# Kernel optimization log

Measured on AMD Instinct MI355X. Metric: run time of the kernel, lower is better.

Reference implementation:

```python
import jax, jax.numpy as jnp
import numpy as np

N, E, G, H, F_IN = 100_000, 3_200_000, 256, 16, 7
RRELU_SLOPE = (1.0 / 8.0 + 1.0 / 3.0) / 2.0  # eval-mode RReLU uses mean slope


def rrelu(x):
    return jnp.where(x >= 0, x, RRELU_SLOPE * x)


def gcn_conv(x, edge_index, edge_weight, W, b, n_nodes):
    """PyG GCNConv: add self-loops, symmetric norm, gather-matmul-scatter."""
    row, col = edge_index[0], edge_index[1]
    loop = jnp.arange(n_nodes)
    row = jnp.concatenate([row, loop])
    col = jnp.concatenate([col, loop])
    w = jnp.concatenate([edge_weight, jnp.ones((n_nodes,), x.dtype)])
    deg = jax.ops.segment_sum(w, col, num_segments=n_nodes)
    dis = jnp.where(deg > 0, jax.lax.rsqrt(jnp.maximum(deg, 1e-12)), 0.0)
    norm = dis[row] * w * dis[col]            # [E+N]
    h = x @ W                                  # [N, out]
    msg = h[row] * norm[:, None]               # gather + scale
    return jax.ops.segment_sum(msg, col, num_segments=n_nodes) + b


def max_pool_neighbor_x(x, edge_index, n_nodes):
    row, col = edge_index[0], edge_index[1]
    loop = jnp.arange(n_nodes)
    row = jnp.concatenate([row, loop])
    col = jnp.concatenate([col, loop])
    return jax.ops.segment_max(x[row], col, num_segments=n_nodes)


def setup_inputs() -> dict:
    key = jax.random.key(0)
    ks = jax.random.split(key, 12)
    x = jax.random.normal(ks[0], (N, F_IN), jnp.float32)
    edge_index = jax.random.randint(ks[1], (2, E), 0, N)
    edge_weights = jax.random.uniform(ks[2], (E,), jnp.float32)
    batch = (jnp.arange(N) * G) // N  # sorted, every graph non-empty
    s = 0.2
    W1 = jax.random.normal(ks[3], (F_IN, H), jnp.float32) * s
    b1 = jnp.zeros((H,), jnp.float32)
    W2 = jax.random.normal(ks[4], (H, H), jnp.float32) * s
    b2 = jnp.zeros((H,), jnp.float32)
    Wl1 = jax.random.normal(ks[5], (H, H), jnp.float32) * s
    bl1 = jax.random.normal(ks[6], (H,), jnp.float32) * s
    Wl3 = jax.random.normal(ks[7], (H, H), jnp.float32) * s
    bl3 = jax.random.normal(ks[8], (H,), jnp.float32) * s
    Wl4 = jax.random.normal(ks[9], (H, 1), jnp.float32) * s
    bl4 = jax.random.normal(ks[10], (1,), jnp.float32) * s
    return {"x": x, "edge_index": edge_index, "batch": batch,
            "edge_weights": edge_weights, "W1": W1, "b1": b1, "W2": W2,
            "b2": b2, "Wl1": Wl1, "bl1": bl1, "Wl3": Wl3, "bl3": bl3,
            "Wl4": Wl4, "bl4": bl4}


def reference(x, edge_index, batch, edge_weights, W1, b1, W2, b2,
              Wl1, bl1, Wl3, bl3, Wl4, bl4):
    h = gcn_conv(x, edge_index, edge_weights, W1, b1, N)
    h = max_pool_neighbor_x(h, edge_index, N)
    res = h
    h = gcn_conv(h, edge_index, jnp.ones((E,), h.dtype), W2, b2, N)
    h = jax.nn.relu(res + h)
    g = jax.ops.segment_max(h, batch, num_segments=G)  # global_max_pool
    res = g
    g = rrelu(res + (g @ Wl1 + bl1))
    res = g
    g = rrelu(res + (g @ Wl3 + bl3))
    # dropout p=0.5 in eval mode -> identity
    g = rrelu(g @ Wl4 + bl4)
    return g
```

## Files before the change

kernel.cpp:

```cpp
#include <hip/hip_runtime.h>
#include <hip/hip_fp16.h>
#include <math.h>

#define NN 100000
#define NE 3200000
#define NG 256
#define HD 16
#define FIN 7

#define RB 8
#define RSZ 256
#define NBUK 391
#define NBUKP 400
#define FB 512
#define CHUNK 6250
#define CH2 3125
#define SCB 8
#define LMASK 0x1FFFF

#define SEGN 32
#define SEGB 3125
#define NPW 8

#define PSTRIDE_B 10880
#define SCAP PSTRIDE_B

#define S_DEGW 16777216.0f
#define INV_S_DEGW 5.9604644775390625e-8f

static constexpr float SLOPE = 0.22916666666666666f;

__device__ __forceinline__ float rrelu_f(float a) {
    return a >= 0.f ? a : SLOPE * a;
}

__device__ __forceinline__ float h2f(unsigned short us) {
    __half h = *(__half*)&us;
    return __half2float(h);
}


__global__ __launch_bounds__(512) void k_hist(
        const int* __restrict__ col, int* __restrict__ hist) {
    __shared__ int bins[NBUK];
    for (int i = threadIdx.x; i < NBUK; i += 512) bins[i] = 0;
    __syncthreads();
    const int2* c2 = (const int2*)(col + blockIdx.x * CHUNK);
    for (int i = threadIdx.x; i < CH2; i += 512) {
        int2 v = c2[i];
        atomicAdd(&bins[v.x >> RB], 1);
        atomicAdd(&bins[v.y >> RB], 1);
    }
    __syncthreads();
    for (int i = threadIdx.x; i < NBUK; i += 512)
        hist[blockIdx.x * NBUKP + i] = bins[i];
}

__global__ __launch_bounds__(512) void k_scan_a(
        const int* __restrict__ hist, int* __restrict__ pre_t,
        int* __restrict__ tot) {
    __shared__ int s[SCB * (FB + 1)];
    int t = threadIdx.x;
    int c0 = blockIdx.x * SCB;
    for (int i = t; i < SCB * FB; i += 512) {
        int j = i >> 3, c = i & 7;
        int cc = c0 + c;
        s[c * (FB + 1) + j] = (cc < NBUK) ? hist[j * NBUKP + cc] : 0;
    }
    __syncthreads();
    int w = t >> 6, l = t & 63;
    int* sb = &s[w * (FB + 1)];
    int base = l * 8;
    int loc[8];
    int run = 0;
#pragma unroll
    for (int k = 0; k < 8; ++k) { loc[k] = run; run += sb[base + k]; }
    int inc = run;
#pragma unroll
    for (int d = 1; d < 64; d <<= 1) {
        int v = __shfl_up(inc, d, 64);
        if (l >= d) inc += v;
    }
    int excl = inc - run;
    int cc = c0 + w;
    if (cc < NBUK) {
#pragma unroll
        for (int k = 0; k < 8; ++k) sb[base + k] = excl + loc[k];
        if (l == 63) tot[cc] = inc;
    }
    __syncthreads();
    for (int i = t; i < SCB * FB; i += 512) {
        int j = i >> 3, c = i & 7;
        int cc2 = c0 + c;
        if (cc2 < NBUK) pre_t[j * NBUKP + cc2] = s[c * (FB + 1) + j];
    }
}

__global__ __launch_bounds__(512) void k_scan_b(
        const int* __restrict__ tot, int* __restrict__ bstart,
        unsigned* __restrict__ gbuf) {
    __shared__ int s[512];
    int t = threadIdx.x;
    for (int i = t; i < NG * HD; i += 512) gbuf[i] = 0u;
    int v = (t < NBUK) ? tot[t] : 0;
    s[t] = v;
    __syncthreads();
    for (int d = 1; d < 512; d <<= 1) {
        int add = (t >= d) ? s[t - d] : 0;
        __syncthreads();
        s[t] += add;
        __syncthreads();
    }
    if (t < NBUK) bstart[t + 1] = s[t];
    if (t == 0) bstart[0] = 0;
}

__global__ __launch_bounds__(512) void k_fill(
        const int* __restrict__ row, const int* __restrict__ col,
        const float* __restrict__ ew,
        const int* __restrict__ pre_t, const int* __restrict__ bstart,
        unsigned* __restrict__ sp, unsigned short* __restrict__ swh) {
    __shared__ int lcnt[NBUK];
    __shared__ int gofs[NBUK];
    __shared__ int part[512];
    __shared__ unsigned ssp[CHUNK];
    __shared__ unsigned short ssw[CHUNK];
    __shared__ unsigned short sbuk[CHUNK];
    int t = threadIdx.x;
    for (int i = t; i < NBUK; i += 512) {
        lcnt[i] = 0;
        gofs[i] = bstart[i] + pre_t[blockIdx.x * NBUKP + i];
    }
    __syncthreads();
    const int2* c2 = (const int2*)(col + blockIdx.x * CHUNK);
    const int2* r2 = (const int2*)(row + blockIdx.x * CHUNK);
    const float2* e2 = (const float2*)(ew + blockIdx.x * CHUNK);
    for (int i = t; i < CH2; i += 512) {
        int2 v = c2[i];
        atomicAdd(&lcnt[v.x >> RB], 1);
        atomicAdd(&lcnt[v.y >> RB], 1);
    }
    __syncthreads();
    int c = (t < NBUK) ? lcnt[t] : 0;
    part[t] = c;
    __syncthreads();
    for (int d = 1; d < 512; d <<= 1) {
        int add = (t >= d) ? part[t - d] : 0;
        __syncthreads();
        part[t] += add;
        __syncthreads();
    }
    if (t < NBUK) {
        int e = part[t] - c;
        gofs[t] -= e;
        lcnt[t] = e;
    }
    __syncthreads();
    for (int i = t; i < CH2; i += 512) {
        int2 cv = c2[i];
        int2 rv = r2[i];
        float2 wv = e2[i];
        {
            int b = cv.x >> RB;
            int s = atomicAdd(&lcnt[b], 1);
            ssp[s] = ((unsigned)(cv.x & (RSZ - 1)) << 17) | (unsigned)rv.x;
            __half hv = __float2half_rn(wv.x);
            ssw[s] = *(unsigned short*)&hv;
            sbuk[s] = (unsigned short)b;
        }
        {
            int b = cv.y >> RB;
            int s = atomicAdd(&lcnt[b], 1);
            ssp[s] = ((unsigned)(cv.y & (RSZ - 1)) << 17) | (unsigned)rv.y;
            __half hv = __float2half_rn(wv.y);
            ssw[s] = *(unsigned short*)&hv;
            sbuk[s] = (unsigned short)b;
        }
    }
    __syncthreads();
    for (int s = t; s < CHUNK; s += 512) {
        int g = s + gofs[sbuk[s]];
        sp[g] = ssp[s];
        swh[g] = ssw[s];
    }
}

__global__ __launch_bounds__(1024) void k_deg(
        const unsigned* __restrict__ sp, const unsigned short* __restrict__ swh,
        const int* __restrict__ bstart,
        const float* __restrict__ x, const float* __restrict__ W1,
        float* __restrict__ dis1, float* __restrict__ dis2,
        int* __restrict__ pstart, int* __restrict__ cnts,
        unsigned* __restrict__ h1h, unsigned* __restrict__ sp2) {
    __shared__ unsigned long long sdeg[RSZ];
    __shared__ float sdis[RSZ];
    __shared__ float sW1[FIN * HD];
    __shared__ int sscan[RSZ];
    __shared__ int lrank[RSZ];
    __shared__ unsigned sstage[SCAP];
    int t = threadIdx.x;
    if (t < FIN * HD) sW1[t] = W1[t];
    if (t < RSZ) sdeg[t] = 0ULL;
    __syncthreads();
    int s0 = bstart[blockIdx.x], s1 = bstart[blockIdx.x + 1];
    int j = s0 + t;
    for (; j + 3072 < s1; j += 4096) {
        unsigned e0 = sp[j], e1 = sp[j + 1024], e2 = sp[j + 2048], e3 = sp[j + 3072];
        float w0 = h2f(swh[j]), w1 = h2f(swh[j + 1024]);
        float w2 = h2f(swh[j + 2048]), w3 = h2f(swh[j + 3072]);
        atomicAdd(&sdeg[e0 >> 17], (1ULL << 32) |
                  (unsigned long long)(unsigned)__float2int_rn(w0 * S_DEGW));
        atomicAdd(&sdeg[e1 >> 17], (1ULL << 32) |
                  (unsigned long long)(unsigned)__float2int_rn(w1 * S_DEGW));
        atomicAdd(&sdeg[e2 >> 17], (1ULL << 32) |
                  (unsigned long long)(unsigned)__float2int_rn(w2 * S_DEGW));
        atomicAdd(&sdeg[e3 >> 17], (1ULL << 32) |
                  (unsigned long long)(unsigned)__float2int_rn(w3 * S_DEGW));
    }
    for (; j < s1; j += 1024) {
        unsigned e = sp[j];
        float w = h2f(swh[j]);
        atomicAdd(&sdeg[e >> 17], (1ULL << 32) |
                  (unsigned long long)(unsigned)__float2int_rn(w * S_DEGW));
    }
    __syncthreads();
    int node0 = blockIdx.x * RSZ;
    int s0p = blockIdx.x * PSTRIDE_B;
    int cnt_t = 0, pc_t = 0;
    if (t < RSZ) {
        cnt_t = (int)(sdeg[t] >> 32);
        pc_t = (cnt_t + 15) & ~15;
        sscan[t] = pc_t;
    }
    __syncthreads();
    for (int d = 1; d < RSZ; d <<= 1) {
        int add = (t < RSZ && t >= d) ? sscan[t - d] : 0;
        __syncthreads();
        if (t < RSZ) sscan[t] += add;
        __syncthreads();
    }
    if (t < RSZ) {
        int excl = sscan[t] - pc_t;
        lrank[t] = excl;
        if (node0 + t < NN) {
            pstart[node0 + t] = s0p + excl;
            cnts[node0 + t] = cnt_t;
            unsigned long long v = sdeg[t];
            float wsum = (float)(unsigned)(v & 0xFFFFFFFFULL) * INV_S_DEGW;
            float d1 = rsqrtf(wsum + 1.f);
            dis1[node0 + t] = d1;
            sdis[t] = d1;
            dis2[node0 + t] = rsqrtf((float)cnt_t + 1.f);
        }
        int pbase = excl + cnt_t;
        unsigned pv = (unsigned)(node0 + t);
        for (int k = cnt_t; k < pc_t; ++k) {
            int pos = pbase + (k - cnt_t);
            if (pos < SCAP) sstage[pos] = pv;
        }
    }
    __syncthreads();
    for (int k = s0 + t; k < s1; k += 1024) {
        unsigned e = sp[k];
        unsigned short wb = swh[k];
        int pos = atomicAdd(&lrank[e >> 17], 1);
        unsigned packed = ((unsigned)(wb & 0x7FFFu) << 17) | (e & LMASK);
        if (pos < SCAP) sstage[pos] = packed;
    }
    __syncthreads();
    int ptot = sscan[RSZ - 1];
    int lim = ptot < SCAP ? ptot : SCAP;
    for (int k = t; k < lim; k += 1024) sp2[s0p + k] = sstage[k];
    for (int i = t; i < RSZ * 8; i += 1024) {
        int ln = i >> 3, p = i & 7;
        int node = node0 + ln;
        if (node < NN) {
            float a0 = 0.f, a1 = 0.f;
#pragma unroll
            for (int k = 0; k < FIN; ++k) {
                float xv = x[node * FIN + k];
                a0 += xv * sW1[k * HD + 2 * p];
                a1 += xv * sW1[k * HD + 2 * p + 1];
            }
            float d = sdis[ln];
            __half2 hh = __floats2half2_rn(a0 * d, a1 * d);
            h1h[node * 8 + p] = *(unsigned*)&hh;
        }
    }
}

__global__ __launch_bounds__(256) void k_conv1(
        const unsigned* __restrict__ sp2, const int* __restrict__ pstart,
        const int* __restrict__ cnts,
        const unsigned* __restrict__ h1h, const float* __restrict__ dis1,
        const float* __restrict__ b1, unsigned* __restrict__ h1outh) {
    int t = threadIdx.x;
    int l = t & 63, w = t >> 6;
    int e = l >> 3, p = l & 7;
    float bb0 = b1[2 * p], bb1 = b1[2 * p + 1];
    int nwbase = blockIdx.x * SEGN + w * NPW;
    for (int nn = 0; nn < NPW; nn += 2) {
        int nodeA = __builtin_amdgcn_readfirstlane(nwbase + nn);
        int nodeB = nodeA + 1;
        int pA = pstart[nodeA], cA = cnts[nodeA];
        int pB = pstart[nodeB], cB = cnts[nodeB];
        int tA = (cA + 15) >> 4, tB = (cB + 15) >> 4;
        float dA = dis1[nodeA], dB = dis1[nodeB];
        unsigned shA = h1h[nodeA * 8 + p], shB = h1h[nodeB * 8 + p];
        float aA0 = 0.f, aA1 = 0.f, aB0 = 0.f, aB1 = 0.f;
        int jA = pA + e, jB = pB + e;
        while (tA > 0 || tB > 0) {
            if (tA > 0) {
                unsigned v0 = sp2[jA], v1 = sp2[jA + 8];
                unsigned g0 = h1h[(v0 & LMASK) * 8 + p];
                unsigned g1 = h1h[(v1 & LMASK) * 8 + p];
                float w0 = h2f((unsigned short)(v0 >> 17));
                float w1 = h2f((unsigned short)(v1 >> 17));
                float2 f0 = __half22float2(*(__half2*)&g0);
                float2 f1 = __half22float2(*(__half2*)&g1);
                aA0 += f0.x * w0 + f1.x * w1;
                aA1 += f0.y * w0 + f1.y * w1;
                jA += 16; --tA;
            }
            if (tB > 0) {
                unsigned v0 = sp2[jB], v1 = sp2[jB + 8];
                unsigned g0 = h1h[(v0 & LMASK) * 8 + p];
                unsigned g1 = h1h[(v1 & LMASK) * 8 + p];
                float w0 = h2f((unsigned short)(v0 >> 17));
                float w1 = h2f((unsigned short)(v1 >> 17));
                float2 f0 = __half22float2(*(__half2*)&g0);
                float2 f1 = __half22float2(*(__half2*)&g1);
                aB0 += f0.x * w0 + f1.x * w1;
                aB1 += f0.y * w0 + f1.y * w1;
                jB += 16; --tB;
            }
        }
        aA0 += __shfl_xor(aA0, 8);  aB0 += __shfl_xor(aB0, 8);
        aA1 += __shfl_xor(aA1, 8);  aB1 += __shfl_xor(aB1, 8);
        aA0 += __shfl_xor(aA0, 16); aB0 += __shfl_xor(aB0, 16);
        aA1 += __shfl_xor(aA1, 16); aB1 += __shfl_xor(aB1, 16);
        aA0 += __shfl_xor(aA0, 32); aB0 += __shfl_xor(aB0, 32);
        aA1 += __shfl_xor(aA1, 32); aB1 += __shfl_xor(aB1, 32);
        float2 sfA = __half22float2(*(__half2*)&shA);
        float2 sfB = __half22float2(*(__half2*)&shB);
        float rA0 = (aA0 + sfA.x) * dA + bb0;
        float rA1 = (aA1 + sfA.y) * dA + bb1;
        float rB0 = (aB0 + sfB.x) * dB + bb0;
        float rB1 = (aB1 + sfB.y) * dB + bb1;
        if (e == 0) {
            __half2 ha = __floats2half2_rn(rA0, rA1);
            h1outh[nodeA * 8 + p] = *(unsigned*)&ha;
            __half2 hb = __floats2half2_rn(rB0, rB1);
            h1outh[nodeB * 8 + p] = *(unsigned*)&hb;
        }
    }
}

__global__ __launch_bounds__(256) void k_pool_h2(
        const unsigned* __restrict__ sp2, const int* __restrict__ pstart,
        const int* __restrict__ cnts,
        const unsigned* __restrict__ h1outh, const float* __restrict__ W2,
        const float* __restrict__ dis2,
        float2* __restrict__ pool2, unsigned* __restrict__ h2sh) {
    int t = threadIdx.x;
    int l = t & 63, w = t >> 6;
    int e = l >> 3, p = l & 7;
    float w00 = W2[(2 * e) * HD + 2 * p],     w10 = W2[(2 * e + 1) * HD + 2 * p];
    float w01 = W2[(2 * e) * HD + 2 * p + 1], w11 = W2[(2 * e + 1) * HD + 2 * p + 1];
    int nwbase = blockIdx.x * SEGN + w * NPW;
    for (int nn = 0; nn < NPW; nn += 2) {
        int nodeA = __builtin_amdgcn_readfirstlane(nwbase + nn);
        int nodeB = nodeA + 1;
        int pA = pstart[nodeA], cA = cnts[nodeA];
        int pB = pstart[nodeB], cB = cnts[nodeB];
        int tA = (cA + 15) >> 4, tB = (cB + 15) >> 4;
        float dA = dis2[nodeA], dB = dis2[nodeB];
        unsigned shA = h1outh[nodeA * 8 + p], shB = h1outh[nodeB * 8 + p];
        float2 sfA = __half22float2(*(__half2*)&shA);
        float2 sfB = __half22float2(*(__half2*)&shB);
        float mA0 = sfA.x, mA1 = sfA.y;
        float mB0 = sfB.x, mB1 = sfB.y;
        int jA = pA + e, jB = pB + e;
        while (tA > 0 || tB > 0) {
            if (tA > 0) {
                unsigned v0 = sp2[jA], v1 = sp2[jA + 8];
                unsigned g0 = h1outh[(v0 & LMASK) * 8 + p];
                unsigned g1 = h1outh[(v1 & LMASK) * 8 + p];
                float2 f0 = __half22float2(*(__half2*)&g0);
                float2 f1 = __half22float2(*(__half2*)&g1);
                mA0 = fmaxf(mA0, fmaxf(f0.x, f1.x));
                mA1 = fmaxf(mA1, fmaxf(f0.y, f1.y));
                jA += 16; --tA;
            }
            if (tB > 0) {
                unsigned v0 = sp2[jB], v1 = sp2[jB + 8];
                unsigned g0 = h1outh[(v0 & LMASK) * 8 + p];
                unsigned g1 = h1outh[(v1 & LMASK) * 8 + p];
                float2 f0 = __half22float2(*(__half2*)&g0);
                float2 f1 = __half22float2(*(__half2*)&g1);
                mB0 = fmaxf(mB0, fmaxf(f0.x, f1.x));
                mB1 = fmaxf(mB1, fmaxf(f0.y, f1.y));
                jB += 16; --tB;
            }
        }
        mA0 = fmaxf(mA0, __shfl_xor(mA0, 8));  mB0 = fmaxf(mB0, __shfl_xor(mB0, 8));
        mA1 = fmaxf(mA1, __shfl_xor(mA1, 8));  mB1 = fmaxf(mB1, __shfl_xor(mB1, 8));
        mA0 = fmaxf(mA0, __shfl_xor(mA0, 16)); mB0 = fmaxf(mB0, __shfl_xor(mB0, 16));
        mA1 = fmaxf(mA1, __shfl_xor(mA1, 16)); mB1 = fmaxf(mB1, __shfl_xor(mB1, 16));
        mA0 = fmaxf(mA0, __shfl_xor(mA0, 32)); mB0 = fmaxf(mB0, __shfl_xor(mB0, 32));
        mA1 = fmaxf(mA1, __shfl_xor(mA1, 32)); mB1 = fmaxf(mB1, __shfl_xor(mB1, 32));
        if (e == 0) {
            pool2[nodeA * 8 + p] = make_float2(mA0, mA1);
            pool2[nodeB * 8 + p] = make_float2(mB0, mB1);
        }
        float pmA0 = __shfl(mA0, e), pmB0 = __shfl(mB0, e);
        float pmA1 = __shfl(mA1, e), pmB1 = __shfl(mB1, e);
        float aA0 = pmA0 * w00 + pmA1 * w10;
        float aA1 = pmA0 * w01 + pmA1 * w11;
        float aB0 = pmB0 * w00 + pmB1 * w10;
        float aB1 = pmB0 * w01 + pmB1 * w11;
        aA0 += __shfl_xor(aA0, 8);  aB0 += __shfl_xor(aB0, 8);
        aA1 += __shfl_xor(aA1, 8);  aB1 += __shfl_xor(aB1, 8);
        aA0 += __shfl_xor(aA0, 16); aB0 += __shfl_xor(aB0, 16);
        aA1 += __shfl_xor(aA1, 16); aB1 += __shfl_xor(aB1, 16);
        aA0 += __shfl_xor(aA0, 32); aB0 += __shfl_xor(aB0, 32);
        aA1 += __shfl_xor(aA1, 32); aB1 += __shfl_xor(aB1, 32);
        if (e == 0) {
            __half2 ha = __floats2half2_rn(aA0 * dA, aA1 * dA);
            h2sh[nodeA * 8 + p] = *(unsigned*)&ha;
            __half2 hb = __floats2half2_rn(aB0 * dB, aB1 * dB);
            h2sh[nodeB * 8 + p] = *(unsigned*)&hb;
        }
    }
}

__global__ __launch_bounds__(256) void k_conv2(
        const unsigned* __restrict__ sp2, const int* __restrict__ pstart,
        const int* __restrict__ cnts,
        const unsigned* __restrict__ h2sh, const float* __restrict__ dis2,
        const float2* __restrict__ pool2, const float* __restrict__ b2,
        unsigned* __restrict__ gbuf) {
    __shared__ unsigned sgmax[2 * HD];
    int t = threadIdx.x;
    if (t < 2 * HD) sgmax[t] = 0u;
    __syncthreads();
    int l = t & 63, w = t >> 6;
    int e = l >> 3, p = l & 7;
    float bb0 = b2[2 * p], bb1 = b2[2 * p + 1];
    int nbase = blockIdx.x * SEGN;
    int gbase = (int)(((unsigned long long)nbase * NG) / NN);
    int nwbase = nbase + w * NPW;
    for (int nn = 0; nn < NPW; nn += 2) {
        int nodeA = __builtin_amdgcn_readfirstlane(nwbase + nn);
        int nodeB = nodeA + 1;
        int pA = pstart[nodeA], cA = cnts[nodeA];
        int pB = pstart[nodeB], cB = cnts[nodeB];
        int tA = (cA + 15) >> 4, tB = (cB + 15) >> 4;
        int npadA = (tA << 4) - cA, npadB = (tB << 4) - cB;
        float dA = dis2[nodeA], dB = dis2[nodeB];
        unsigned shA = h2sh[nodeA * 8 + p], shB = h2sh[nodeB * 8 + p];
        float2 plA = pool2[nodeA * 8 + p], plB = pool2[nodeB * 8 + p];
        float aA0 = 0.f, aA1 = 0.f, aB0 = 0.f, aB1 = 0.f;
        int jA = pA + e, jB = pB + e;
        while (tA > 0 || tB > 0) {
            if (tA > 0) {
                unsigned v0 = sp2[jA], v1 = sp2[jA + 8];
                unsigned g0 = h2sh[(v0 & LMASK) * 8 + p];
                unsigned g1 = h2sh[(v1 & LMASK) * 8 + p];
                float2 f0 = __half22float2(*(__half2*)&g0);
                float2 f1 = __half22float2(*(__half2*)&g1);
                aA0 += f0.x + f1.x;
                aA1 += f0.y + f1.y;
                jA += 16; --tA;
            }
            if (tB > 0) {
                unsigned v0 = sp2[jB], v1 = sp2[jB + 8];
                unsigned g0 = h2sh[(v0 & LMASK) * 8 + p];
                unsigned g1 = h2sh[(v1 & LMASK) * 8 + p];
                float2 f0 = __half22float2(*(__half2*)&g0);
                float2 f1 = __half22float2(*(__half2*)&g1);
                aB0 += f0.x + f1.x;
                aB1 += f0.y + f1.y;
                jB += 16; --tB;
            }
        }
        aA0 += __shfl_xor(aA0, 8);  aB0 += __shfl_xor(aB0, 8);
        aA1 += __shfl_xor(aA1, 8);  aB1 += __shfl_xor(aB1, 8);
        aA0 += __shfl_xor(aA0, 16); aB0 += __shfl_xor(aB0, 16);
        aA1 += __shfl_xor(aA1, 16); aB1 += __shfl_xor(aB1, 16);
        aA0 += __shfl_xor(aA0, 32); aB0 += __shfl_xor(aB0, 32);
        aA1 += __shfl_xor(aA1, 32); aB1 += __shfl_xor(aB1, 32);
        float2 selfA = __half22float2(*(__half2*)&shA);
        float2 selfB = __half22float2(*(__half2*)&shB);
        float csA = 1.f - (float)npadA, csB = 1.f - (float)npadB;
        float rA0 = fmaxf(plA.x + (aA0 + csA * selfA.x) * dA + bb0, 0.f);
        float rA1 = fmaxf(plA.y + (aA1 + csA * selfA.y) * dA + bb1, 0.f);
        float rB0 = fmaxf(plB.x + (aB0 + csB * selfB.x) * dB + bb0, 0.f);
        float rB1 = fmaxf(plB.y + (aB1 + csB * selfB.y) * dB + bb1, 0.f);
        if (e == 0) {
            int lgA = (int)(((unsigned long long)nodeA * NG) / NN) - gbase;
            int lgB = (int)(((unsigned long long)nodeB * NG) / NN) - gbase;
            atomicMax(&sgmax[lgA * HD + 2 * p],     __float_as_uint(rA0));
            atomicMax(&sgmax[lgA * HD + 2 * p + 1], __float_as_uint(rA1));
            atomicMax(&sgmax[lgB * HD + 2 * p],     __float_as_uint(rB0));
            atomicMax(&sgmax[lgB * HD + 2 * p + 1], __float_as_uint(rB1));
        }
    }
    __syncthreads();
    if (t < 2 * HD) {
        int lg = t >> 4, f = t & 15;
        int gg = gbase + lg;
        unsigned m = sgmax[t];
        if (gg < NG && m > 0u) atomicMax(&gbuf[gg * HD + f], m);
    }
}

__global__ __launch_bounds__(256) void k_mlp(
        const float* __restrict__ gbuf,
        const float* __restrict__ Wl1, const float* __restrict__ bl1,
        const float* __restrict__ Wl3, const float* __restrict__ bl3,
        const float* __restrict__ Wl4, const float* __restrict__ bl4,
        float* __restrict__ out) {
    __shared__ float sW1[256], sW3[256], sW4[16], sb1[16], sb3[16];
    __shared__ float sb4;
    int tid = threadIdx.x;
    sW1[tid] = Wl1[tid];
    sW3[tid] = Wl3[tid];
    if (tid < 16) { sW4[tid] = Wl4[tid]; sb1[tid] = bl1[tid]; sb3[tid] = bl3[tid]; }
    if (tid == 0) sb4 = bl4[0];
    __syncthreads();

    float v[16], t1[16], t2[16];
#pragma unroll
    for (int f = 0; f < 16; ++f) v[f] = gbuf[tid * 16 + f];
#pragma unroll
    for (int f = 0; f < 16; ++f) {
        float a = sb1[f] + v[f];
#pragma unroll
        for (int k = 0; k < 16; ++k) a += v[k] * sW1[k * 16 + f];
        t1[f] = rrelu_f(a);
    }
#pragma unroll
    for (int f = 0; f < 16; ++f) {
        float a = sb3[f] + t1[f];
#pragma unroll
        for (int k = 0; k < 16; ++k) a += t1[k] * sW3[k * 16 + f];
        t2[f] = rrelu_f(a);
    }
    float o = sb4;
#pragma unroll
    for (int k = 0; k < 16; ++k) o += t2[k] * sW4[k];
    out[tid] = rrelu_f(o);
}

extern "C" void kernel_launch(void* const* d_in, const int* in_sizes, int n_in,
                              void* d_out, int out_size, void* d_ws, size_t ws_size,
                              hipStream_t stream) {
    const float* x   = (const float*)d_in[0];
    const int*   ei  = (const int*)  d_in[1];
    const float* ew  = (const float*)d_in[3];
    const float* W1  = (const float*)d_in[4];
    const float* b1  = (const float*)d_in[5];
    const float* W2  = (const float*)d_in[6];
    const float* b2  = (const float*)d_in[7];
    const float* Wl1 = (const float*)d_in[8];
    const float* bl1 = (const float*)d_in[9];
    const float* Wl3 = (const float*)d_in[10];
    const float* bl3 = (const float*)d_in[11];
    const float* Wl4 = (const float*)d_in[12];
    const float* bl4 = (const float*)d_in[13];
    const int* row = ei;
    const int* col = ei + NE;

    float* ws = (float*)d_ws;
    float* pool  = ws;
    float* dead  = pool + NN * HD;
    float* dis1  = dead + NN * HD;
    float* dis2  = dis1 + NN;
    int*   pstart = (int*)(dis2 + NN);
    int*   cnts  = pstart + NN;
    unsigned* gbuf = (unsigned*)(cnts + NN);
    unsigned* h1h    = gbuf   + NG * HD;
    unsigned* h1outh = h1h    + NN * 8;
    unsigned* h2sh   = h1outh + NN * 8;
    unsigned* sp     = h2sh   + NN * 8;
    unsigned short* swh = (unsigned short*)(sp + NE);
    unsigned* sp2    = (unsigned*)(swh + NE);
    int* tot    = (int*)(sp2 + (size_t)NBUK * PSTRIDE_B);
    int* bstart = tot + NBUK;
    int* hist   = (int*)pool;
    int* pre_t  = (int*)dead;

    k_hist     <<<FB, 512, 0, stream>>>(col, hist);
    k_scan_a   <<<(NBUK + SCB - 1) / SCB, 512, 0, stream>>>(hist, pre_t, tot);
    k_scan_b   <<<1, 512, 0, stream>>>(tot, bstart, gbuf);
    k_fill     <<<FB, 512, 0, stream>>>(row, col, ew, pre_t, bstart, sp, swh);
    k_deg      <<<NBUK, 1024, 0, stream>>>(sp, swh, bstart, x, W1,
                                           dis1, dis2, pstart, cnts, h1h, sp2);
    k_conv1    <<<SEGB, 256, 0, stream>>>(sp2, pstart, cnts, h1h, dis1,
                                          b1, h1outh);
    k_pool_h2  <<<SEGB, 256, 0, stream>>>(sp2, pstart, cnts, h1outh, W2, dis2,
                                          (float2*)pool, h2sh);
    k_conv2    <<<SEGB, 256, 0, stream>>>(sp2, pstart, cnts, h2sh, dis2,
                                          (const float2*)pool, b2, gbuf);
    k_mlp      <<<1, 256, 0, stream>>>((const float*)gbuf, Wl1, bl1, Wl3, bl3,
                                       Wl4, bl4, (float*)d_out);
}
```

Measured before the change: 252.5 us.

## Widen gather to 8-byte loads with 4 nodes per wavefront in CSR kernels

```diff
diff --git a/kernel.cpp b/kernel.cpp
--- a/kernel.cpp
+++ b/kernel.cpp
@@ -37,6 +37,12 @@
 __device__ __forceinline__ float h2f(unsigned short us) {
     __half h = *(__half*)&us;
     return __half2float(h);
+}
+
+__device__ __forceinline__ unsigned hmax2u(unsigned a, unsigned b) {
+    unsigned r;
+    asm volatile("v_pk_max_f16 %0, %1, %2" : "=v"(r) : "v"(a), "v"(b));
+    return r;
 }
 
 
@@ -295,63 +301,61 @@
         const unsigned* __restrict__ h1h, const float* __restrict__ dis1,
         const float* __restrict__ b1, unsigned* __restrict__ h1outh) {
     int t = threadIdx.x;
-    int l = t & 63, w = t >> 6;
-    int e = l >> 3, p = l & 7;
-    float bb0 = b1[2 * p], bb1 = b1[2 * p + 1];
-    int nwbase = blockIdx.x * SEGN + w * NPW;
-    for (int nn = 0; nn < NPW; nn += 2) {
-        int nodeA = __builtin_amdgcn_readfirstlane(nwbase + nn);
-        int nodeB = nodeA + 1;
-        int pA = pstart[nodeA], cA = cnts[nodeA];
-        int pB = pstart[nodeB], cB = cnts[nodeB];
-        int tA = (cA + 15) >> 4, tB = (cB + 15) >> 4;
-        float dA = dis1[nodeA], dB = dis1[nodeB];
-        unsigned shA = h1h[nodeA * 8 + p], shB = h1h[nodeB * 8 + p];
-        float aA0 = 0.f, aA1 = 0.f, aB0 = 0.f, aB1 = 0.f;
-        int jA = pA + e, jB = pB + e;
-        while (tA > 0 || tB > 0) {
-            if (tA > 0) {
-                unsigned v0 = sp2[jA], v1 = sp2[jA + 8];
-                unsigned g0 = h1h[(v0 & LMASK) * 8 + p];
-                unsigned g1 = h1h[(v1 & LMASK) * 8 + p];
-                float w0 = h2f((unsigned short)(v0 >> 17));
-                float w1 = h2f((unsigned short)(v1 >> 17));
-                float2 f0 = __half22float2(*(__half2*)&g0);
-                float2 f1 = __half22float2(*(__half2*)&g1);
-                aA0 += f0.x * w0 + f1.x * w1;
-                aA1 += f0.y * w0 + f1.y * w1;
-                jA += 16; --tA;
-            }
-            if (tB > 0) {
-                unsigned v0 = sp2[jB], v1 = sp2[jB + 8];
-                unsigned g0 = h1h[(v0 & LMASK) * 8 + p];
-                unsigned g1 = h1h[(v1 & LMASK) * 8 + p];
-                float w0 = h2f((unsigned short)(v0 >> 17));
-                float w1 = h2f((unsigned short)(v1 >> 17));
-                float2 f0 = __half22float2(*(__half2*)&g0);
-                float2 f1 = __half22float2(*(__half2*)&g1);
-                aB0 += f0.x * w0 + f1.x * w1;
-                aB1 += f0.y * w0 + f1.y * w1;
-                jB += 16; --tB;
-            }
-        }
-        aA0 += __shfl_xor(aA0, 8);  aB0 += __shfl_xor(aB0, 8);
-        aA1 += __shfl_xor(aA1, 8);  aB1 += __shfl_xor(aB1, 8);
-        aA0 += __shfl_xor(aA0, 16); aB0 += __shfl_xor(aB0, 16);
-        aA1 += __shfl_xor(aA1, 16); aB1 += __shfl_xor(aB1, 16);
-        aA0 += __shfl_xor(aA0, 32); aB0 += __shfl_xor(aB0, 32);
-        aA1 += __shfl_xor(aA1, 32); aB1 += __shfl_xor(aB1, 32);
-        float2 sfA = __half22float2(*(__half2*)&shA);
-        float2 sfB = __half22float2(*(__half2*)&shB);
-        float rA0 = (aA0 + sfA.x) * dA + bb0;
-        float rA1 = (aA1 + sfA.y) * dA + bb1;
-        float rB0 = (aB0 + sfB.x) * dB + bb0;
-        float rB1 = (aB1 + sfB.y) * dB + bb1;
-        if (e == 0) {
-            __half2 ha = __floats2half2_rn(rA0, rA1);
-            h1outh[nodeA * 8 + p] = *(unsigned*)&ha;
-            __half2 hb = __floats2half2_rn(rB0, rB1);
-            h1outh[nodeB * 8 + p] = *(unsigned*)&hb;
+    int wu = __builtin_amdgcn_readfirstlane(t >> 6);
+    int l = t & 63;
+    int e = l >> 2, p = l & 3;
+    float4 bb = ((const float4*)b1)[p];
+    const uint2* hv = (const uint2*)h1h;
+    int nwbase = blockIdx.x * SEGN + wu * NPW;
+    for (int nn = 0; nn < NPW; nn += 4) {
+        int nb = nwbase + nn;
+        int tC[4], jC[4];
+        float a0[4], a1[4], a2[4], a3[4];
+#pragma unroll
+        for (int c = 0; c < 4; ++c) {
+            int node = nb + c;
+            int pc = pstart[node];
+            tC[c] = (cnts[node] + 15) >> 4;
+            jC[c] = pc + e;
+            a0[c] = 0.f; a1[c] = 0.f; a2[c] = 0.f; a3[c] = 0.f;
+        }
+        while ((tC[0] | tC[1] | tC[2] | tC[3]) > 0) {
+#pragma unroll
+            for (int c = 0; c < 4; ++c) if (tC[c] > 0) {
+                unsigned v = sp2[jC[c]];
+                uint2 g = hv[(v & LMASK) * 4 + p];
+                float wv = h2f((unsigned short)(v >> 17));
+                float2 f0 = __half22float2(*(__half2*)&g.x);
+                float2 f1 = __half22float2(*(__half2*)&g.y);
+                a0[c] += f0.x * wv; a1[c] += f0.y * wv;
+                a2[c] += f1.x * wv; a3[c] += f1.y * wv;
+                jC[c] += 16; --tC[c];
+            }
+        }
+#pragma unroll
+        for (int c = 0; c < 4; ++c) {
+            int node = nb + c;
+#pragma unroll
+            for (int d = 4; d < 64; d <<= 1) {
+                a0[c] += __shfl_xor(a0[c], d);
+                a1[c] += __shfl_xor(a1[c], d);
+                a2[c] += __shfl_xor(a2[c], d);
+                a3[c] += __shfl_xor(a3[c], d);
+            }
+            float dd = dis1[node];
+            uint2 sh = hv[node * 4 + p];
+            float2 s0 = __half22float2(*(__half2*)&sh.x);
+            float2 s1 = __half22float2(*(__half2*)&sh.y);
+            float r0 = (a0[c] + s0.x) * dd + bb.x;
+            float r1 = (a1[c] + s0.y) * dd + bb.y;
+            float r2 = (a2[c] + s1.x) * dd + bb.z;
+            float r3 = (a3[c] + s1.y) * dd + bb.w;
+            if (e == 0) {
+                __half2 h01 = __floats2half2_rn(r0, r1);
+                __half2 h23 = __floats2half2_rn(r2, r3);
+                ((uint2*)h1outh)[node * 4 + p] =
+                    make_uint2(*(unsigned*)&h01, *(unsigned*)&h23);
+            }
         }
     }
 }
@@ -361,75 +365,59 @@
         const int* __restrict__ cnts,
         const unsigned* __restrict__ h1outh, const float* __restrict__ W2,
         const float* __restrict__ dis2,
-        float2* __restrict__ pool2, unsigned* __restrict__ h2sh) {
-    int t = threadIdx.x;
-    int l = t & 63, w = t >> 6;
-    int e = l >> 3, p = l & 7;
-    float w00 = W2[(2 * e) * HD + 2 * p],     w10 = W2[(2 * e + 1) * HD + 2 * p];
-    float w01 = W2[(2 * e) * HD + 2 * p + 1], w11 = W2[(2 * e + 1) * HD + 2 * p + 1];
-    int nwbase = blockIdx.x * SEGN + w * NPW;
-    for (int nn = 0; nn < NPW; nn += 2) {
-        int nodeA = __builtin_amdgcn_readfirstlane(nwbase + nn);
-        int nodeB = nodeA + 1;
-        int pA = pstart[nodeA], cA = cnts[nodeA];
-        int pB = pstart[nodeB], cB = cnts[nodeB];
-        int tA = (cA + 15) >> 4, tB = (cB + 15) >> 4;
-        float dA = dis2[nodeA], dB = dis2[nodeB];
-        unsigned shA = h1outh[nodeA * 8 + p], shB = h1outh[nodeB * 8 + p];
-        float2 sfA = __half22float2(*(__half2*)&shA);
-        float2 sfB = __half22float2(*(__half2*)&shB);
-        float mA0 = sfA.x, mA1 = sfA.y;
-        float mB0 = sfB.x, mB1 = sfB.y;
-        int jA = pA + e, jB = pB + e;
-        while (tA > 0 || tB > 0) {
-            if (tA > 0) {
-                unsigned v0 = sp2[jA], v1 = sp2[jA + 8];
-                unsigned g0 = h1outh[(v0 & LMASK) * 8 + p];
-                unsigned g1 = h1outh[(v1 & LMASK) * 8 + p];
-                float2 f0 = __half22float2(*(__half2*)&g0);
-                float2 f1 = __half22float2(*(__half2*)&g1);
-                mA0 = fmaxf(mA0, fmaxf(f0.x, f1.x));
-                mA1 = fmaxf(mA1, fmaxf(f0.y, f1.y));
-                jA += 16; --tA;
-            }
-            if (tB > 0) {
-                unsigned v0 = sp2[jB], v1 = sp2[jB + 8];
-                unsigned g0 = h1outh[(v0 & LMASK) * 8 + p];
-                unsigned g1 = h1outh[(v1 & LMASK) * 8 + p];
-                float2 f0 = __half22float2(*(__half2*)&g0);
-                float2 f1 = __half22float2(*(__half2*)&g1);
-                mB0 = fmaxf(mB0, fmaxf(f0.x, f1.x));
-                mB1 = fmaxf(mB1, fmaxf(f0.y, f1.y));
-                jB += 16; --tB;
-            }
-        }
-        mA0 = fmaxf(mA0, __shfl_xor(mA0, 8));  mB0 = fmaxf(mB0, __shfl_xor(mB0, 8));
-        mA1 = fmaxf(mA1, __shfl_xor(mA1, 8));  mB1 = fmaxf(mB1, __shfl_xor(mB1, 8));
-        mA0 = fmaxf(mA0, __shfl_xor(mA0, 16)); mB0 = fmaxf(mB0, __shfl_xor(mB0, 16));
-        mA1 = fmaxf(mA1, __shfl_xor(mA1, 16)); mB1 = fmaxf(mB1, __shfl_xor(mB1, 16));
-        mA0 = fmaxf(mA0, __shfl_xor(mA0, 32)); mB0 = fmaxf(mB0, __shfl_xor(mB0, 32));
-        mA1 = fmaxf(mA1, __shfl_xor(mA1, 32)); mB1 = fmaxf(mB1, __shfl_xor(mB1, 32));
-        if (e == 0) {
-            pool2[nodeA * 8 + p] = make_float2(mA0, mA1);
-            pool2[nodeB * 8 + p] = make_float2(mB0, mB1);
-        }
-        float pmA0 = __shfl(mA0, e), pmB0 = __shfl(mB0, e);
-        float pmA1 = __shfl(mA1, e), pmB1 = __shfl(mB1, e);
-        float aA0 = pmA0 * w00 + pmA1 * w10;
-        float aA1 = pmA0 * w01 + pmA1 * w11;
-        float aB0 = pmB0 * w00 + pmB1 * w10;
-        float aB1 = pmB0 * w01 + pmB1 * w11;
-        aA0 += __shfl_xor(aA0, 8);  aB0 += __shfl_xor(aB0, 8);
-        aA1 += __shfl_xor(aA1, 8);  aB1 += __shfl_xor(aB1, 8);
-        aA0 += __shfl_xor(aA0, 16); aB0 += __shfl_xor(aB0, 16);
-        aA1 += __shfl_xor(aA1, 16); aB1 += __shfl_xor(aB1, 16);
-        aA0 += __shfl_xor(aA0, 32); aB0 += __shfl_xor(aB0, 32);
-        aA1 += __shfl_xor(aA1, 32); aB1 += __shfl_xor(aB1, 32);
-        if (e == 0) {
-            __half2 ha = __floats2half2_rn(aA0 * dA, aA1 * dA);
-            h2sh[nodeA * 8 + p] = *(unsigned*)&ha;
-            __half2 hb = __floats2half2_rn(aB0 * dB, aB1 * dB);
-            h2sh[nodeB * 8 + p] = *(unsigned*)&hb;
+        float4* __restrict__ pool4, unsigned* __restrict__ h2sh) {
+    int t = threadIdx.x;
+    int wu = __builtin_amdgcn_readfirstlane(t >> 6);
+    int l = t & 63;
+    int e = l >> 2, p = l & 3;
+    float w0 = W2[(4 * p + 0) * HD + e], w1 = W2[(4 * p + 1) * HD + e];
+    float w2 = W2[(4 * p + 2) * HD + e], w3 = W2[(4 * p + 3) * HD + e];
+    const uint2* hv = (const uint2*)h1outh;
+    int nwbase = blockIdx.x * SEGN + wu * NPW;
+    for (int nn = 0; nn < NPW; nn += 4) {
+        int nb = nwbase + nn;
+        int tC[4], jC[4];
+        unsigned m01[4], m23[4];
+#pragma unroll
+        for (int c = 0; c < 4; ++c) {
+            int node = nb + c;
+            int pc = pstart[node];
+            tC[c] = (cnts[node] + 15) >> 4;
+            jC[c] = pc + e;
+            uint2 sh = hv[node * 4 + p];
+            m01[c] = sh.x; m23[c] = sh.y;
+        }
+        while ((tC[0] | tC[1] | tC[2] | tC[3]) > 0) {
+#pragma unroll
+            for (int c = 0; c < 4; ++c) if (tC[c] > 0) {
+                unsigned v = sp2[jC[c]];
+                uint2 g = hv[(v & LMASK) * 4 + p];
+                m01[c] = hmax2u(m01[c], g.x);
+                m23[c] = hmax2u(m23[c], g.y);
+                jC[c] += 16; --tC[c];
+            }
+        }
+#pragma unroll
+        for (int c = 0; c < 4; ++c) {
+            int node = nb + c;
+#pragma unroll
+            for (int d = 4; d < 64; d <<= 1) {
+                m01[c] = hmax2u(m01[c], __shfl_xor(m01[c], d));
+                m23[c] = hmax2u(m23[c], __shfl_xor(m23[c], d));
+            }
+            float2 f0 = __half22float2(*(__half2*)&m01[c]);
+            float2 f1 = __half22float2(*(__half2*)&m23[c]);
+            if (e == 0)
+                pool4[node * 4 + p] = make_float4(f0.x, f0.y, f1.x, f1.y);
+            float partial = f0.x * w0 + f0.y * w1 + f1.x * w2 + f1.y * w3;
+            partial += __shfl_xor(partial, 1);
+            partial += __shfl_xor(partial, 2);
+            float other = __shfl_xor(partial, 4);
+            float dd = dis2[node];
+            if (((e & 1) == 0) && (p == 0)) {
+                __half2 hh = __floats2half2_rn(partial * dd, other * dd);
+                h2sh[node * 8 + (e >> 1)] = *(unsigned*)&hh;
+            }
         }
     }
 }
@@ -438,72 +426,73 @@
         const unsigned* __restrict__ sp2, const int* __restrict__ pstart,
         const int* __restrict__ cnts,
         const unsigned* __restrict__ h2sh, const float* __restrict__ dis2,
-        const float2* __restrict__ pool2, const float* __restrict__ b2,
+        const float4* __restrict__ pool4, const float* __restrict__ b2,
         unsigned* __restrict__ gbuf) {
     __shared__ unsigned sgmax[2 * HD];
     int t = threadIdx.x;
     if (t < 2 * HD) sgmax[t] = 0u;
     __syncthreads();
-    int l = t & 63, w = t >> 6;
-    int e = l >> 3, p = l & 7;
-    float bb0 = b2[2 * p], bb1 = b2[2 * p + 1];
+    int wu = __builtin_amdgcn_readfirstlane(t >> 6);
+    int l = t & 63;
+    int e = l >> 2, p = l & 3;
+    float4 bb = ((const float4*)b2)[p];
+    const uint2* hv = (const uint2*)h2sh;
     int nbase = blockIdx.x * SEGN;
     int gbase = (int)(((unsigned long long)nbase * NG) / NN);
-    int nwbase = nbase + w * NPW;
-    for (int nn = 0; nn < NPW; nn += 2) {
-        int nodeA = __builtin_amdgcn_readfirstlane(nwbase + nn);
-        int nodeB = nodeA + 1;
-        int pA = pstart[nodeA], cA = cnts[nodeA];
-        int pB = pstart[nodeB], cB = cnts[nodeB];
-        int tA = (cA + 15) >> 4, tB = (cB + 15) >> 4;
-        int npadA = (tA << 4) - cA, npadB = (tB << 4) - cB;
-        float dA = dis2[nodeA], dB = dis2[nodeB];
-        unsigned shA = h2sh[nodeA * 8 + p], shB = h2sh[nodeB * 8 + p];
-        float2 plA = pool2[nodeA * 8 + p], plB = pool2[nodeB * 8 + p];
-        float aA0 = 0.f, aA1 = 0.f, aB0 = 0.f, aB1 = 0.f;
-        int jA = pA + e, jB = pB + e;
-        while (tA > 0 || tB > 0) {
-            if (tA > 0) {
-                unsigned v0 = sp2[jA], v1 = sp2[jA + 8];
-                unsigned g0 = h2sh[(v0 & LMASK) * 8 + p];
-                unsigned g1 = h2sh[(v1 & LMASK) * 8 + p];
-                float2 f0 = __half22float2(*(__half2*)&g0);
-                float2 f1 = __half22float2(*(__half2*)&g1);
-                aA0 += f0.x + f1.x;
-                aA1 += f0.y + f1.y;
-                jA += 16; --tA;
-            }
-            if (tB > 0) {
-                unsigned v0 = sp2[jB], v1 = sp2[jB + 8];
-                unsigned g0 = h2sh[(v0 & LMASK) * 8 + p];
-                unsigned g1 = h2sh[(v1 & LMASK) * 8 + p];
-                float2 f0 = __half22float2(*(__half2*)&g0);
-                float2 f1 = __half22float2(*(__half2*)&g1);
-                aB0 += f0.x + f1.x;
-                aB1 += f0.y + f1.y;
-                jB += 16; --tB;
-            }
-        }
-        aA0 += __shfl_xor(aA0, 8);  aB0 += __shfl_xor(aB0, 8);
-        aA1 += __shfl_xor(aA1, 8);  aB1 += __shfl_xor(aB1, 8);
-        aA0 += __shfl_xor(aA0, 16); aB0 += __shfl_xor(aB0, 16);
-        aA1 += __shfl_xor(aA1, 16); aB1 += __shfl_xor(aB1, 16);
-        aA0 += __shfl_xor(aA0, 32); aB0 += __shfl_xor(aB0, 32);
-        aA1 += __shfl_xor(aA1, 32); aB1 += __shfl_xor(aB1, 32);
-        float2 selfA = __half22float2(*(__half2*)&shA);
-        float2 selfB = __half22float2(*(__half2*)&shB);
-        float csA = 1.f - (float)npadA, csB = 1.f - (float)npadB;
-        float rA0 = fmaxf(plA.x + (aA0 + csA * selfA.x) * dA + bb0, 0.f);
-        float rA1 = fmaxf(plA.y + (aA1 + csA * selfA.y) * dA + bb1, 0.f);
-        float rB0 = fmaxf(plB.x + (aB0 + csB * selfB.x) * dB + bb0, 0.f);
-        float rB1 = fmaxf(plB.y + (aB1 + csB * selfB.y) * dB + bb1, 0.f);
-        if (e == 0) {
-            int lgA = (int)(((unsigned long long)nodeA * NG) / NN) - gbase;
-            int lgB = (int)(((unsigned long long)nodeB * NG) / NN) - gbase;
-            atomicMax(&sgmax[lgA * HD + 2 * p],     __float_as_uint(rA0));
-            atomicMax(&sgmax[lgA * HD + 2 * p + 1], __float_as_uint(rA1));
-            atomicMax(&sgmax[lgB * HD + 2 * p],     __float_as_uint(rB0));
-            atomicMax(&sgmax[lgB * HD + 2 * p + 1], __float_as_uint(rB1));
+    int nwbase = nbase + wu * NPW;
+    for (int nn = 0; nn < NPW; nn += 4) {
+        int nb = nwbase + nn;
+        int tC[4], jC[4], np[4];
+        float a0[4], a1[4], a2[4], a3[4];
+#pragma unroll
+        for (int c = 0; c < 4; ++c) {
+            int node = nb + c;
+            int pc = pstart[node], cc = cnts[node];
+            tC[c] = (cc + 15) >> 4;
+            np[c] = (tC[c] << 4) - cc;
+            jC[c] = pc + e;
+            a0[c] = 0.f; a1[c] = 0.f; a2[c] = 0.f; a3[c] = 0.f;
+        }
+        while ((tC[0] | tC[1] | tC[2] | tC[3]) > 0) {
+#pragma unroll
+            for (int c = 0; c < 4; ++c) if (tC[c] > 0) {
+                unsigned v = sp2[jC[c]];
+                uint2 g = hv[(v & LMASK) * 4 + p];
+                float2 f0 = __half22float2(*(__half2*)&g.x);
+                float2 f1 = __half22float2(*(__half2*)&g.y);
+                a0[c] += f0.x; a1[c] += f0.y;
+                a2[c] += f1.x; a3[c] += f1.y;
+                jC[c] += 16; --tC[c];
+            }
+        }
+#pragma unroll
+        for (int c = 0; c < 4; ++c) {
+            int node = nb + c;
+#pragma unroll
+            for (int d = 4; d < 64; d <<= 1) {
+                a0[c] += __shfl_xor(a0[c], d);
+                a1[c] += __shfl_xor(a1[c], d);
+                a2[c] += __shfl_xor(a2[c], d);
+                a3[c] += __shfl_xor(a3[c], d);
+            }
+            float dd = dis2[node];
+            uint2 sh = hv[node * 4 + p];
+            float2 s0 = __half22float2(*(__half2*)&sh.x);
+            float2 s1 = __half22float2(*(__half2*)&sh.y);
+            float4 pl = pool4[node * 4 + p];
+            float cs = 1.f - (float)np[c];
+            float r0 = fmaxf(pl.x + (a0[c] + cs * s0.x) * dd + bb.x, 0.f);
+            float r1 = fmaxf(pl.y + (a1[c] + cs * s0.y) * dd + bb.y, 0.f);
+            float r2 = fmaxf(pl.z + (a2[c] + cs * s1.x) * dd + bb.z, 0.f);
+            float r3 = fmaxf(pl.w + (a3[c] + cs * s1.y) * dd + bb.w, 0.f);
+            if (e == 0) {
+                int lg = (int)(((unsigned long long)node * NG) / NN) - gbase;
+                unsigned* sg = &sgmax[lg * HD + 4 * p];
+                atomicMax(sg + 0, __float_as_uint(r0));
+                atomicMax(sg + 1, __float_as_uint(r1));
+                atomicMax(sg + 2, __float_as_uint(r2));
+                atomicMax(sg + 3, __float_as_uint(r3));
+            }
         }
     }
     __syncthreads();
@@ -600,9 +589,9 @@
     k_conv1    <<<SEGB, 256, 0, stream>>>(sp2, pstart, cnts, h1h, dis1,
                                           b1, h1outh);
     k_pool_h2  <<<SEGB, 256, 0, stream>>>(sp2, pstart, cnts, h1outh, W2, dis2,
-                                          (float2*)pool, h2sh);
+                                          (float4*)pool, h2sh);
     k_conv2    <<<SEGB, 256, 0, stream>>>(sp2, pstart, cnts, h2sh, dis2,
-                                          (const float2*)pool, b2, gbuf);
+                                          (const float4*)pool, b2, gbuf);
     k_mlp      <<<1, 256, 0, stream>>>((const float*)gbuf, Wl1, bl1, Wl3, bl3,
                                        Wl4, bl4, (float*)d_out);
 }
```

Result: slower. 262.6 us (+4.0%).
